# Optimization experiments

Hardware: AMD Instinct MI355X
Metric: run time of the kernel (lower is better)

## Reference

```python
import jax, jax.numpy as jnp
import numpy as np

N = 100000
MUL = 16


def _build_cg():
    # Real-basis Clebsch-Gordan (Wigner-3j-style) coefficients, shape (2l1+1, 2l2+1, 2lo+1),
    # each normalized to unit Frobenius norm per output component (e3nn component normalization).
    eps = np.zeros((3, 3, 3), np.float32)
    for a, b, c in [(0, 1, 2), (1, 2, 0), (2, 0, 1)]:
        eps[a, b, c] = 1.0
        eps[a, c, b] = -1.0
    s2 = np.float32(1.0 / np.sqrt(2.0))
    q = np.zeros((5, 3, 3), np.float32)  # l=2 real harmonics: xy, yz, 3z^2-r^2, xz, x^2-y^2
    q[0, 0, 1] = q[0, 1, 0] = s2
    q[1, 1, 2] = q[1, 2, 1] = s2
    q[2] = np.diag([-1.0, -1.0, 2.0]).astype(np.float32) / np.sqrt(6.0)
    q[3, 0, 2] = q[3, 2, 0] = s2
    q[4] = np.diag([1.0, -1.0, 0.0]).astype(np.float32) * s2
    cg000 = jnp.ones((1, 1, 1), jnp.float32)                                   # 0e x 0e -> 0e
    cg011 = jnp.asarray(np.eye(3, dtype=np.float32)[None])                      # 0e x 1o -> 1o
    cg110 = jnp.asarray((np.eye(3, dtype=np.float32) / np.sqrt(3.0))[:, :, None])  # 1o x 1o -> 0e
    cg111 = jnp.asarray(eps * s2)                                               # 1o x 1o -> 1e
    cg112 = jnp.asarray(np.transpose(q, (1, 2, 0)))                             # 1o x 1o -> 2e
    return cg000, cg011, cg110, cg111, cg112


def _path(x1, x2, cg, w, alpha):
    # 'uvw' tensor-product path: out[z,w,m] = alpha * sum_{u,v,i,j} x1[z,u,i] x2[z,v,j] cg[i,j,m] w[u,v,w]
    # Contraction order chosen to keep the largest intermediate at [z,u,w,j].
    t = jnp.einsum('zvj,uvw->zuwj', x2, w)
    s = jnp.einsum('zui,zuwj->zwij', x1, t)
    return alpha * jnp.einsum('zwij,ijm->zwm', s, cg)


def _tensor_square(x, w0, w1, w2, w3, w4):
    n = x.shape[0]
    x0 = x[:, :MUL].reshape(n, MUL, 1)       # 16x0e
    x1 = x[:, MUL:].reshape(n, MUL, 3)       # 16x1o
    cg000, cg011, cg110, cg111, cg112 = _build_cg()
    a2 = 1.0 / np.sqrt(MUL * MUL * 2.0)      # 0e output receives 2 paths
    a1 = 1.0 / np.sqrt(MUL * MUL * 1.0)
    o_0e = _path(x0, x0, cg000, w0, a2) + _path(x1, x1, cg110, w2, a2)
    o_1o = _path(x0, x1, cg011, w1, a1)
    o_1e = _path(x1, x1, cg111, w3, a1)
    o_2e = _path(x1, x1, cg112, w4, a1)
    return jnp.concatenate([o.reshape(n, -1) for o in (o_0e, o_1o, o_1e, o_2e)], axis=1)


def setup_inputs() -> dict:
    key = jax.random.key(0)
    kx, k0, k1, k2, k3, k4 = jax.random.split(key, 6)
    return {
        'x': jax.random.normal(kx, (N, MUL * 1 + MUL * 3), jnp.float32),
        'w0': jax.random.normal(k0, (MUL, MUL, MUL), jnp.float32),
        'w1': jax.random.normal(k1, (MUL, MUL, MUL), jnp.float32),
        'w2': jax.random.normal(k2, (MUL, MUL, MUL), jnp.float32),
        'w3': jax.random.normal(k3, (MUL, MUL, MUL), jnp.float32),
        'w4': jax.random.normal(k4, (MUL, MUL, MUL), jnp.float32),
    }


def reference(x, w0, w1, w2, w3, w4):
    return _tensor_square(x, w0, w1, w2, w3, w4)
```

## Files before the change

### kernel.cpp

```cpp
#include <hip/hip_runtime.h>
#include <hip/hip_bf16.h>

typedef __attribute__((ext_vector_type(8))) short short8;
typedef __attribute__((ext_vector_type(4))) float float4v;
typedef __attribute__((ext_vector_type(2))) float float2v;
typedef __attribute__((ext_vector_type(4))) unsigned uint4v;

#define S_A 0.04419417382415922f
#define S_B 0.025515518153991442f
#define S_C 0.0625f

static __device__ __forceinline__ unsigned pkbf(float a, float b) {
#if __has_builtin(__builtin_amdgcn_cvt_pk_bf16_f32)
    auto v = __builtin_amdgcn_cvt_pk_bf16_f32(a, b);
    return __builtin_bit_cast(unsigned, v);
#else
    unsigned ua = __builtin_bit_cast(unsigned, a);
    unsigned ub = __builtin_bit_cast(unsigned, b);
    ua += 0x7fffu + ((ua >> 16) & 1u);
    ub += 0x7fffu + ((ub >> 16) & 1u);
    return __builtin_amdgcn_perm(ub, ua, 0x07060302);
#endif
}

__global__ void wprep_kernel(const float* __restrict__ wA, const float* __restrict__ wB,
                             const float* __restrict__ wC, const float* __restrict__ wD,
                             const float* __restrict__ wE, unsigned short* __restrict__ wout)
{
    int e = blockIdx.x * 256 + threadIdx.x;
    if (e >= 5 * 4096) return;
    int p = e >> 12;
    int rem = e & 4095;
    const float* wp = (p == 0) ? wA : (p == 1) ? wB : (p == 2) ? wC : (p == 3) ? wD : wE;
    unsigned u = __builtin_bit_cast(unsigned, wp[rem]);
    u += 0x7fffu + ((u >> 16) & 1u);
    int k = rem >> 4, w = rem & 15;
    int c = k >> 5, kk = k & 31;
    int lane = ((kk >> 3) << 4) | w;
    int j = kk & 7;
    wout[(((c * 5 + p) * 64 + lane) << 3) | j] = (unsigned short)(u >> 16);
}

template<int G>
static __device__ __forceinline__ int pathof(int i) {
    if constexpr (G == 0) return (i == 0) ? 0 : (i == 1) ? 1 : 4;
    if constexpr (G == 1) return (i == 0) ? 2 : (i == 1) ? 3 : 4;
    return (i == 0) ? 3 : 4;
}

template<int G>
static __device__ __forceinline__ void run_group(
    const float* __restrict__ xr, int l, const short8* __restrict__ wbase,
    float* __restrict__ out, long long z0)
{
    const int r  = l & 15;
    const int g  = l >> 4;
    const int v0 = (g & 1) * 8;
    const int uo = g >> 1;

    float2v Xv[4], Yv[4], Zv[4];
    float2v A0v[4];
    {
        float b[24];
        #pragma unroll
        for (int q = 0; q < 6; q++)
            *(float4v*)&b[q * 4] = *(const float4v*)(xr + 16 + v0 * 3 + q * 4);
        #pragma unroll
        for (int t = 0; t < 4; t++) {
            Xv[t] = (float2v){b[6 * t + 0], b[6 * t + 3]};
            Yv[t] = (float2v){b[6 * t + 1], b[6 * t + 4]};
            Zv[t] = (float2v){b[6 * t + 2], b[6 * t + 5]};
        }
        if constexpr (G == 0) {
            float a[8];
            #pragma unroll
            for (int q = 0; q < 2; q++)
                *(float4v*)&a[q * 4] = *(const float4v*)(xr + v0 + q * 4);
            #pragma unroll
            for (int t = 0; t < 4; t++) A0v[t] = (float2v){a[2 * t], a[2 * t + 1]};
        }
    }

    constexpr int NS = (G == 1) ? 5 : 4;
    constexpr int NP = (G == 2) ? 2 : 3;

    float4v acc[NS];
    #pragma unroll
    for (int s = 0; s < NS; s++) acc[s] = (float4v){0.f, 0.f, 0.f, 0.f};

    short8 wcur[NP], wnxt[NP];
    #pragma unroll
    for (int i = 0; i < NP; i++) wcur[i] = wbase[(0 * 5 + pathof<G>(i)) * 64 + l];

    #pragma unroll
    for (int c = 0; c < 8; c++) {
        if (c < 7) {
            #pragma unroll
            for (int i = 0; i < NP; i++) wnxt[i] = wbase[((c + 1) * 5 + pathof<G>(i)) * 64 + l];
        }

        const int u = c * 2 + uo;
        float u0 = 0.f, ux = 0.f, uy, uz;
        if constexpr (G != 2) u0 = xr[u];
        if constexpr (G != 1) ux = xr[16 + u * 3 + 0];
        uy = xr[16 + u * 3 + 1];
        uz = xr[16 + u * 3 + 2];

        unsigned fri[NS][4];
        #pragma unroll
        for (int t = 0; t < 4; t++) {
            const float2v X = Xv[t], Y = Yv[t], Z = Zv[t];
            if constexpr (G == 0) {
                float2v b0  = u0 * A0v[t];
                float2v p00 = ux * X, p11 = uy * Y, p22 = uz * Z;
                float2v t01 = p00 + p11;
                float2v b1  = t01 + p22;
                float2v b10 = 2.0f * p22 - t01;
                float2v b12 = p00 - p11;
                fri[0][t] = pkbf(b0.x, b0.y);
                fri[1][t] = pkbf(b1.x, b1.y);
                fri[2][t] = pkbf(b10.x, b10.y);
                fri[3][t] = pkbf(b12.x, b12.y);
            }
            if constexpr (G == 1) {
                float2v b2 = u0 * X, b3 = u0 * Y, b4 = u0 * Z;
                float2v p12 = uy * Z;
                float2v b5 = p12 - uz * Y;
                float2v b9 = p12 + uz * Y;
                fri[0][t] = pkbf(b2.x, b2.y);
                fri[1][t] = pkbf(b3.x, b3.y);
                fri[2][t] = pkbf(b4.x, b4.y);
                fri[3][t] = pkbf(b5.x, b5.y);
                fri[4][t] = pkbf(b9.x, b9.y);
            }
            if constexpr (G == 2) {
                float2v p01 = ux * Y;
                float2v b7  = p01 - uy * X;
                float2v b8  = p01 + uy * X;
                float2v p02 = ux * Z;
                float2v b6  = uz * X - p02;
                float2v b11 = p02 + uz * X;
                fri[0][t] = pkbf(b6.x, b6.y);
                fri[1][t] = pkbf(b7.x, b7.y);
                fri[2][t] = pkbf(b8.x, b8.y);
                fri[3][t] = pkbf(b11.x, b11.y);
            }
        }

        #pragma unroll
        for (int s = 0; s < NS; s++) {
            short8 frm = __builtin_bit_cast(short8, *(uint4v*)fri[s]);
            int wi;
            if constexpr (G == 0) wi = (s == 0) ? 0 : (s == 1) ? 1 : 2;
            if constexpr (G == 1) wi = (s <= 2) ? 0 : (s == 3) ? 1 : 2;
            if constexpr (G == 2) wi = (s <= 1) ? 0 : 1;
            acc[s] = __builtin_amdgcn_mfma_f32_16x16x32_bf16(frm, wcur[wi], acc[s], 0, 0, 0);
        }

        #pragma unroll
        for (int i = 0; i < NP; i++) wcur[i] = wnxt[i];
    }

    const int w = r;
    float* outp = out + (z0 + g * 4) * 192;
    #pragma unroll
    for (int reg = 0; reg < 4; reg++) {
        float* rowp = outp + reg * 192;
        if constexpr (G == 0) {
            rowp[w]               = S_A * acc[0][reg] + S_B * acc[1][reg];
            rowp[112 + w * 5 + 2] = S_B * acc[2][reg];
            rowp[112 + w * 5 + 4] = S_A * acc[3][reg];
        }
        if constexpr (G == 1) {
            rowp[16 + w * 3 + 0]  = S_C * acc[0][reg];
            rowp[16 + w * 3 + 1]  = S_C * acc[1][reg];
            rowp[16 + w * 3 + 2]  = S_C * acc[2][reg];
            rowp[64 + w * 3 + 0]  = S_A * acc[3][reg];
            rowp[112 + w * 5 + 1] = S_A * acc[4][reg];
        }
        if constexpr (G == 2) {
            rowp[64 + w * 3 + 1]  = S_A * acc[0][reg];
            rowp[64 + w * 3 + 2]  = S_A * acc[1][reg];
            rowp[112 + w * 5 + 0] = S_A * acc[2][reg];
            rowp[112 + w * 5 + 3] = S_A * acc[3][reg];
        }
    }
}

__global__ __launch_bounds__(192, 4)
void tsq_kernel(const float* __restrict__ x,
                const unsigned short* __restrict__ wfrag,
                float* __restrict__ out,
                int nrows)
{
    __shared__ __attribute__((aligned(16))) float xlds[16 * 68];

    const int tid = threadIdx.x;
    const long long z0 = (long long)blockIdx.x * 16;

    {
        const float* xg = x + z0 * 64;
        {
            int f = tid * 4;
            int row = f >> 6, col = f & 63;
            float4v v = {0.f, 0.f, 0.f, 0.f};
            if (z0 + row < nrows) v = *(const float4v*)(xg + f);
            *(float4v*)&xlds[row * 68 + col] = v;
        }
        if (tid < 64) {
            int f = 768 + tid * 4;
            int row = f >> 6, col = f & 63;
            float4v v = {0.f, 0.f, 0.f, 0.f};
            if (z0 + row < nrows) v = *(const float4v*)(xg + f);
            *(float4v*)&xlds[row * 68 + col] = v;
        }
    }
    __syncthreads();
    if (z0 >= nrows) return;

    const int wave = tid >> 6;
    const int l = tid & 63;
    const float* xr = &xlds[(l & 15) * 68];
    const short8* wbase = (const short8*)wfrag;

    if      (wave == 0) run_group<0>(xr, l, wbase, out, z0);
    else if (wave == 1) run_group<1>(xr, l, wbase, out, z0);
    else                run_group<2>(xr, l, wbase, out, z0);
}

extern "C" void kernel_launch(void* const* d_in, const int* in_sizes, int n_in,
                              void* d_out, int out_size, void* d_ws, size_t ws_size,
                              hipStream_t stream) {
    const float* x  = (const float*)d_in[0];
    const float* w0 = (const float*)d_in[1];
    const float* w1 = (const float*)d_in[2];
    const float* w2 = (const float*)d_in[3];
    const float* w3 = (const float*)d_in[4];
    const float* w4 = (const float*)d_in[5];
    float* out = (float*)d_out;
    unsigned short* wfrag = (unsigned short*)d_ws;
    (void)ws_size; (void)n_in; (void)out_size;

    const int nrows = in_sizes[0] / 64;
    const int nblocks = (nrows + 15) / 16;

    wprep_kernel<<<dim3(80), dim3(256), 0, stream>>>(w0, w2, w1, w3, w4, wfrag);
    tsq_kernel<<<dim3(nblocks), dim3(192), 0, stream>>>(x, wfrag, out, nrows);
}
```

Baseline: 137.6 us.

## Stage bf16 weight fragments in LDS and process two 16-row tiles per block

Each block now copies the whole 40 KB prepared bf16 weight-fragment table into shared memory and reads MFMA B-operands from LDS instead of global memory. The block grows to 384 threads covering 32 rows, so six waves share one weight copy. The register double-buffering of weight fragments is dropped because LDS latency is short. The price is a 40 KB per-block global-to-LDS copy and higher LDS use per block, which may cap occupancy below the requested launch bound.

```diff
diff --git a/kernel.cpp b/kernel.cpp
--- a/kernel.cpp
+++ b/kernel.cpp
@@ -88,16 +88,11 @@
     #pragma unroll
     for (int s = 0; s < NS; s++) acc[s] = (float4v){0.f, 0.f, 0.f, 0.f};
 
-    short8 wcur[NP], wnxt[NP];
-    #pragma unroll
-    for (int i = 0; i < NP; i++) wcur[i] = wbase[(0 * 5 + pathof<G>(i)) * 64 + l];
-
     #pragma unroll
     for (int c = 0; c < 8; c++) {
-        if (c < 7) {
-            #pragma unroll
-            for (int i = 0; i < NP; i++) wnxt[i] = wbase[((c + 1) * 5 + pathof<G>(i)) * 64 + l];
-        }
+        short8 wf[NP];
+        #pragma unroll
+        for (int i = 0; i < NP; i++) wf[i] = wbase[(c * 5 + pathof<G>(i)) * 64 + l];
 
         const int u = c * 2 + uo;
         float u0 = 0.f, ux = 0.f, uy, uz;
@@ -154,11 +149,8 @@
             if constexpr (G == 0) wi = (s == 0) ? 0 : (s == 1) ? 1 : 2;
             if constexpr (G == 1) wi = (s <= 2) ? 0 : (s == 3) ? 1 : 2;
             if constexpr (G == 2) wi = (s <= 1) ? 0 : 1;
-            acc[s] = __builtin_amdgcn_mfma_f32_16x16x32_bf16(frm, wcur[wi], acc[s], 0, 0, 0);
-        }
-
-        #pragma unroll
-        for (int i = 0; i < NP; i++) wcur[i] = wnxt[i];
+            acc[s] = __builtin_amdgcn_mfma_f32_16x16x32_bf16(frm, wf[wi], acc[s], 0, 0, 0);
+        }
     }
 
     const int w = r;
@@ -187,32 +179,38 @@
     }
 }
 
-__global__ __launch_bounds__(192, 4)
+__global__ __launch_bounds__(384, 5)
 void tsq_kernel(const float* __restrict__ x,
                 const unsigned short* __restrict__ wfrag,
                 float* __restrict__ out,
                 int nrows)
 {
-    __shared__ __attribute__((aligned(16))) float xlds[16 * 68];
+    __shared__ __attribute__((aligned(16))) unsigned short wlds[5 * 4096];
+    __shared__ __attribute__((aligned(16))) float xlds[32 * 68];
 
     const int tid = threadIdx.x;
-    const long long z0 = (long long)blockIdx.x * 16;
-
+    const long long z0 = (long long)blockIdx.x * 32;
+
+    {
+        const uint4v* src = (const uint4v*)wfrag;
+        uint4v* dst = (uint4v*)wlds;
+        #pragma unroll
+        for (int rr = 0; rr < 6; rr++) dst[rr * 384 + tid] = src[rr * 384 + tid];
+        if (tid < 256) dst[2304 + tid] = src[2304 + tid];
+    }
     {
         const float* xg = x + z0 * 64;
-        {
-            int f = tid * 4;
-            int row = f >> 6, col = f & 63;
-            float4v v = {0.f, 0.f, 0.f, 0.f};
-            if (z0 + row < nrows) v = *(const float4v*)(xg + f);
-            *(float4v*)&xlds[row * 68 + col] = v;
-        }
-        if (tid < 64) {
-            int f = 768 + tid * 4;
-            int row = f >> 6, col = f & 63;
-            float4v v = {0.f, 0.f, 0.f, 0.f};
-            if (z0 + row < nrows) v = *(const float4v*)(xg + f);
-            *(float4v*)&xlds[row * 68 + col] = v;
+        int f = tid * 4;
+        int row = f >> 6, col = f & 63;
+        float4v v = {0.f, 0.f, 0.f, 0.f};
+        if (z0 + row < nrows) v = *(const float4v*)(xg + f);
+        *(float4v*)&xlds[row * 68 + col] = v;
+        if (tid < 128) {
+            f = 1536 + tid * 4;
+            row = f >> 6; col = f & 63;
+            float4v v2 = {0.f, 0.f, 0.f, 0.f};
+            if (z0 + row < nrows) v2 = *(const float4v*)(xg + f);
+            *(float4v*)&xlds[row * 68 + col] = v2;
         }
     }
     __syncthreads();
@@ -220,12 +218,17 @@
 
     const int wave = tid >> 6;
     const int l = tid & 63;
-    const float* xr = &xlds[(l & 15) * 68];
-    const short8* wbase = (const short8*)wfrag;
-
-    if      (wave == 0) run_group<0>(xr, l, wbase, out, z0);
-    else if (wave == 1) run_group<1>(xr, l, wbase, out, z0);
-    else                run_group<2>(xr, l, wbase, out, z0);
+    const int tb = (wave >= 3) ? 1 : 0;
+    const int grp = wave - tb * 3;
+    const long long zb = z0 + tb * 16;
+    if (zb >= nrows) return;
+
+    const float* xr = &xlds[(tb * 16 + (l & 15)) * 68];
+    const short8* wb = (const short8*)wlds;
+
+    if      (grp == 0) run_group<0>(xr, l, wb, out, zb);
+    else if (grp == 1) run_group<1>(xr, l, wb, out, zb);
+    else               run_group<2>(xr, l, wb, out, zb);
 }
 
 extern "C" void kernel_launch(void* const* d_in, const int* in_sizes, int n_in,
@@ -242,8 +245,8 @@
     (void)ws_size; (void)n_in; (void)out_size;
 
     const int nrows = in_sizes[0] / 64;
-    const int nblocks = (nrows + 15) / 16;
+    const int nblocks = (nrows + 31) / 32;
 
     wprep_kernel<<<dim3(80), dim3(256), 0, stream>>>(w0, w2, w1, w3, w4, wfrag);
-    tsq_kernel<<<dim3(nblocks), dim3(192), 0, stream>>>(x, wfrag, out, nrows);
-}
+    tsq_kernel<<<dim3(nblocks), dim3(384), 0, stream>>>(x, wfrag, out, nrows);
+}
```

Measured after the change: 141.4 us. 1.03x slower.
